# Kernel tuning notes

Hardware: AMD Instinct MI355X
Metric: run time of the kernel (lower is better)

Reference implementation:

```python
import jax, jax.numpy as jnp
import numpy as np

N_NODES = 50000
N_EDGES = 800000


def _gcn_conv(x, W, b, src, dst, deg_inv_sqrt, n_nodes):
    # PyG GCNConv: h = x @ W, then symmetric-normalized sum aggregation
    h = x @ W  # [N, F_out]
    norm = deg_inv_sqrt[src] * deg_inv_sqrt[dst]  # [E_aug]
    msg = h[src] * norm[:, None]  # [E_aug, F_out]
    out = jax.ops.segment_sum(msg, dst, num_segments=n_nodes)
    return out + b


def setup_inputs() -> dict:
    key = jax.random.key(0)
    k1, k2, k3, k4 = jax.random.split(key, 4)
    x = jax.random.normal(k1, (N_NODES, 128), dtype=jnp.float32)
    edge_index = jax.random.randint(k2, (2, N_EDGES), 0, N_NODES, dtype=jnp.int64)
    W1 = jax.random.normal(k3, (128, 64), dtype=jnp.float32) * (1.0 / np.sqrt(128))
    b1 = jnp.zeros((64,), dtype=jnp.float32)
    W2 = jax.random.normal(k4, (64, 32), dtype=jnp.float32) * (1.0 / np.sqrt(64))
    b2 = jnp.zeros((32,), dtype=jnp.float32)
    return {"x": x, "edge_index": edge_index, "W1": W1, "b1": b1, "W2": W2, "b2": b2}


def reference(x, edge_index, W1, b1, W2, b2):
    n_nodes = x.shape[0]
    # add self-loops (PyG GCNConv default)
    loop = jnp.arange(n_nodes, dtype=edge_index.dtype)
    src = jnp.concatenate([edge_index[0], loop])
    dst = jnp.concatenate([edge_index[1], loop])
    # symmetric normalization: deg from target index (gcn_norm)
    deg = jax.ops.segment_sum(jnp.ones_like(dst, dtype=x.dtype), dst, num_segments=n_nodes)
    deg_inv_sqrt = jnp.where(deg > 0, jax.lax.rsqrt(jnp.maximum(deg, 1.0)), 0.0)

    h = _gcn_conv(x, W1, b1, src, dst, deg_inv_sqrt, n_nodes)
    h = jax.nn.relu(h)
    # dropout is identity in eval mode (reference runs inference)
    out = _gcn_conv(h, W2, b2, src, dst, deg_inv_sqrt, n_nodes)
    return out
```

## Files before the change

### kernel.cpp

```cpp
#include <hip/hip_runtime.h>
#include <hip/hip_fp16.h>


#define F_IN 128
#define F_MID 64
#define F_OUT 32
#define NBLK 512
#define NGRP 8
#define SUBCAP 1024
#define CAP 8192
#define CAPN 64

#define RFL(x) __builtin_amdgcn_readfirstlane(x)

__device__ __forceinline__ void h8acc(float* a, const uint4& v) {
    const __half2* hp = (const __half2*)&v;
#pragma unroll
    for (int i = 0; i < 4; ++i) {
        float2 f = __half22float2(hp[i]);
        a[2 * i]     += f.x;
        a[2 * i + 1] += f.y;
    }
}

__device__ __forceinline__ void h8unpack(float* f, const uint4& v) {
    const __half2* hp = (const __half2*)&v;
#pragma unroll
    for (int i = 0; i < 4; ++i) {
        float2 t = __half22float2(hp[i]);
        f[2 * i]     = t.x;
        f[2 * i + 1] = t.y;
    }
}

__device__ __forceinline__ uint4 pack8(const float4& a, const float4& b) {
    union { uint4 u; __half2 h[4]; } pk;
    pk.h[0] = __float22half2_rn(make_float2(a.x, a.y));
    pk.h[1] = __float22half2_rn(make_float2(a.z, a.w));
    pk.h[2] = __float22half2_rn(make_float2(b.x, b.y));
    pk.h[3] = __float22half2_rn(make_float2(b.z, b.w));
    return pk.u;
}

__global__ __launch_bounds__(256, 4) void k_build_gemm1(
    const int* __restrict__ src, const int* __restrict__ dst, int E, int chunk,
    int nbuk, int* __restrict__ cursor, int* __restrict__ esort,
    const float* __restrict__ x, const float* __restrict__ W1,
    float* __restrict__ g1raw, int n) {
    __shared__ float xs[64 * 129];
    int t = threadIdx.x;
    if (blockIdx.x < NBLK) {
        int* cnt = (int*)xs;
        int* off = cnt + 256;
        int* lim = off + 256;
        cnt[t] = 0;
        __syncthreads();
        int e0 = blockIdx.x * chunk;
        int e1 = min(E, e0 + chunk);
        for (int e = e0 + t; e < e1; e += 256)
            atomicAdd(&cnt[dst[e] >> 8], 1);
        __syncthreads();
        int g = blockIdx.x & (NGRP - 1);
        if (t < nbuk) {
            int c = cnt[t];
            int base = t * CAP + g * SUBCAP;
            int r = c ? atomicAdd(&cursor[t * NGRP + g], c) : 0;
            off[t] = base + r;
            lim[t] = base + SUBCAP;
        }
        __syncthreads();
        for (int e = e0 + t; e < e1; e += 256) {
            int d = dst[e];
            int b = d >> 8;
            int pos = atomicAdd(&off[b], 1);
            if (pos < lim[b])
                esort[pos] = (src[e] << 8) | (d & 255);
        }
        return;
    }
    int row0 = (blockIdx.x - NBLK) * 64;
    for (int i = t; i < 64 * (F_IN / 4); i += 256) {
        int r = i >> 5, k4 = i & 31;
        int gr = row0 + r;
        float4 v = make_float4(0.f, 0.f, 0.f, 0.f);
        if (gr < n) v = ((const float4*)x)[(size_t)gr * 32 + k4];
        float* p = &xs[r * 129 + k4 * 4];
        p[0] = v.x; p[1] = v.y; p[2] = v.z; p[3] = v.w;
    }
    __syncthreads();
    int w = RFL(t >> 6);
    int r = t & 63;
    const float4* W4 = (const float4*)W1;
    float4 a0 = {0.f,0.f,0.f,0.f}, a1 = a0, a2 = a0, a3 = a0;
#pragma unroll 4
    for (int k = 0; k < F_IN; ++k) {
        float xv = xs[r * 129 + k];
        float4 w0 = W4[k * 16 + w * 4 + 0];
        float4 w1 = W4[k * 16 + w * 4 + 1];
        float4 w2 = W4[k * 16 + w * 4 + 2];
        float4 w3 = W4[k * 16 + w * 4 + 3];
        a0.x += xv * w0.x; a0.y += xv * w0.y; a0.z += xv * w0.z; a0.w += xv * w0.w;
        a1.x += xv * w1.x; a1.y += xv * w1.y; a1.z += xv * w1.z; a1.w += xv * w1.w;
        a2.x += xv * w2.x; a2.y += xv * w2.y; a2.z += xv * w2.z; a2.w += xv * w2.w;
        a3.x += xv * w3.x; a3.y += xv * w3.y; a3.z += xv * w3.z; a3.w += xv * w3.w;
    }
    int gr = row0 + r;
    if (gr < n) {
        float4* G = (float4*)g1raw;
        size_t base = (size_t)gr * 16 + w * 4;
        G[base + 0] = a0; G[base + 1] = a1; G[base + 2] = a2; G[base + 3] = a3;
    }
}

__global__ __launch_bounds__(256) void k_bucket_pad_scale(
    const int* __restrict__ esort, const int* __restrict__ cursor, int n,
    int* __restrict__ deg, int* __restrict__ elist,
    const float* __restrict__ g1raw, uint4* __restrict__ g1h) {
    __shared__ int cur[256];
    int b = blockIdx.x;
    int t = threadIdx.x;
    int node0 = b << 8;
    cur[t] = 0;
    __syncthreads();
#pragma unroll
    for (int g = 0; g < NGRP; ++g) {
        int c = min(cursor[b * NGRP + g], SUBCAP);
        int s0 = b * CAP + g * SUBCAP;
        for (int e = s0 + t; e < s0 + c; e += 256) {
            int p = esort[e];
            int local = p & 255;
            int pos = atomicAdd(&cur[local], 1);
            if (pos < CAPN)
                elist[((node0 + local) << 6) + pos] = p >> 8;
        }
    }
    __syncthreads();
    int node = node0 + t;
    if (node < n) {
        int dg = cur[t];
        deg[node] = dg;
        int padto = dg < 32 ? 32 : min(CAPN, (dg + 7) & ~7);
        for (int p = dg; p < padto; ++p)
            elist[(node << 6) + p] = node;
    }
    for (int i = t; i < 256 * 8; i += 256) {
        int nl = i >> 3, q = i & 7;
        int nd = node0 + nl;
        if (nd < n) {
            float dv = rsqrtf((float)(cur[nl] + 1));
            const float4* G = (const float4*)g1raw + (size_t)nd * 16 + q * 2;
            float4 u = G[0], v = G[1];
            u.x *= dv; u.y *= dv; u.z *= dv; u.w *= dv;
            v.x *= dv; v.y *= dv; v.z *= dv; v.w *= dv;
            g1h[(size_t)nd * 8 + q] = pack8(u, v);
        }
    }
}

__global__ __launch_bounds__(256) void k_gather1(
    const int* __restrict__ deg, const int* __restrict__ elist,
    const uint4* __restrict__ g1h, const float* __restrict__ b1,
    uint4* __restrict__ h16, int n) {
    int wave = RFL(threadIdx.x >> 6);
    int lane = threadIdx.x & 63;
    int q    = lane & 7;
    int slot = lane >> 3;
    int d    = blockIdx.x * 4 + wave;
    if (d >= n) return;
    int base = d << 6;
    int rawdeg = deg[d];
    int s0 = elist[base + slot];
    int s1 = elist[base + 8 + slot];
    int s2 = elist[base + 16 + slot];
    int s3 = elist[base + 24 + slot];
    uint4 v0 = g1h[(size_t)s0 * 8 + q];
    uint4 v1 = g1h[(size_t)s1 * 8 + q];
    uint4 v2 = g1h[(size_t)s2 * 8 + q];
    uint4 v3 = g1h[(size_t)s3 * 8 + q];
    rawdeg = RFL(rawdeg);
    int cnt = min(rawdeg, CAPN);
    float a[8] = {0,0,0,0,0,0,0,0};
    float b[8] = {0,0,0,0,0,0,0,0};
    if (slot == 0) {
        uint4 v = g1h[(size_t)d * 8 + q];
        h8acc(a, v);
    }
    if (slot < cnt)      h8acc(a, v0);
    if (8 + slot < cnt)  h8acc(b, v1);
    if (16 + slot < cnt) h8acc(a, v2);
    if (24 + slot < cnt) h8acc(b, v3);
    if (cnt > 32) {
        int j = 32;
        for (; j + 8 <= cnt; j += 8) {
            int s = elist[base + j + slot];
            uint4 v = g1h[(size_t)s * 8 + q];
            h8acc(a, v);
        }
        if (slot < cnt - j) {
            int s = elist[base + j + slot];
            uint4 v = g1h[(size_t)s * 8 + q];
            h8acc(a, v);
        }
    }
#pragma unroll
    for (int i = 0; i < 8; ++i) a[i] += b[i];
#pragma unroll
    for (int i = 0; i < 8; ++i) a[i] += __shfl_xor(a[i], 8);
#pragma unroll
    for (int i = 0; i < 8; ++i) a[i] += __shfl_xor(a[i], 16);
#pragma unroll
    for (int i = 0; i < 8; ++i) a[i] += __shfl_xor(a[i], 32);
    if (slot == 0) {
        float dv = rsqrtf((float)(rawdeg + 1));
        float4 bv0 = ((const float4*)b1)[q * 2 + 0];
        float4 bv1 = ((const float4*)b1)[q * 2 + 1];
        float4 o0, o1;
        o0.x = fmaxf(a[0] * dv + bv0.x, 0.f);
        o0.y = fmaxf(a[1] * dv + bv0.y, 0.f);
        o0.z = fmaxf(a[2] * dv + bv0.z, 0.f);
        o0.w = fmaxf(a[3] * dv + bv0.w, 0.f);
        o1.x = fmaxf(a[4] * dv + bv1.x, 0.f);
        o1.y = fmaxf(a[5] * dv + bv1.y, 0.f);
        o1.z = fmaxf(a[6] * dv + bv1.z, 0.f);
        o1.w = fmaxf(a[7] * dv + bv1.w, 0.f);
        h16[(size_t)d * 8 + q] = pack8(o0, o1);
    }
}

__global__ __launch_bounds__(256, 4) void k_gemm2(
    const uint4* __restrict__ h16, const float* __restrict__ W2,
    const int* __restrict__ deg, uint4* __restrict__ g2h, int n) {
    __shared__ float hs[64 * 65];
    int tid  = threadIdx.x;
    int row0 = blockIdx.x * 64;
    for (int i = tid; i < 64 * 8; i += 256) {
        int r = i >> 3, q = i & 7;
        int gr = row0 + r;
        float f[8] = {0,0,0,0,0,0,0,0};
        if (gr < n) {
            uint4 v = h16[(size_t)gr * 8 + q];
            h8unpack(f, v);
        }
        float* p = &hs[r * 65 + q * 8];
#pragma unroll
        for (int k = 0; k < 8; ++k) p[k] = f[k];
    }
    __syncthreads();
    int w = RFL(tid >> 6);
    int r = tid & 63;
    const float4* W4 = (const float4*)W2;
    float4 a0 = {0.f,0.f,0.f,0.f}, a1 = a0;
#pragma unroll 4
    for (int k = 0; k < F_MID; ++k) {
        float hv = hs[r * 65 + k];
        float4 w0 = W4[k * 8 + w * 2 + 0];
        float4 w1 = W4[k * 8 + w * 2 + 1];
        a0.x += hv * w0.x; a0.y += hv * w0.y; a0.z += hv * w0.z; a0.w += hv * w0.w;
        a1.x += hv * w1.x; a1.y += hv * w1.y; a1.z += hv * w1.z; a1.w += hv * w1.w;
    }
    int gr = row0 + r;
    if (gr < n) {
        float dv = rsqrtf((float)(deg[gr] + 1));
        a0.x *= dv; a0.y *= dv; a0.z *= dv; a0.w *= dv;
        a1.x *= dv; a1.y *= dv; a1.z *= dv; a1.w *= dv;
        g2h[(size_t)gr * 4 + w] = pack8(a0, a1);
    }
}

__global__ __launch_bounds__(256) void k_gather2(
    const int* __restrict__ deg, const int* __restrict__ elist,
    const uint4* __restrict__ g2h, const float* __restrict__ b2,
    float* __restrict__ out, int n) {
    int wave = RFL(threadIdx.x >> 6);
    int lane = threadIdx.x & 63;
    int q    = lane & 3;
    int slot = lane >> 2;
    int d    = blockIdx.x * 4 + wave;
    if (d >= n) return;
    int base = d << 6;
    int rawdeg = deg[d];
    int s0 = elist[base + slot];
    int s1 = elist[base + 16 + slot];
    uint4 v0 = g2h[(size_t)s0 * 4 + q];
    uint4 v1 = g2h[(size_t)s1 * 4 + q];
    rawdeg = RFL(rawdeg);
    int cnt = min(rawdeg, CAPN);
    float a[8] = {0,0,0,0,0,0,0,0};
    float b[8] = {0,0,0,0,0,0,0,0};
    if (slot == 0) {
        uint4 v = g2h[(size_t)d * 4 + q];
        h8acc(a, v);
    }
    if (slot < cnt)      h8acc(a, v0);
    if (16 + slot < cnt) h8acc(b, v1);
    if (cnt > 32) {
        int j = 32;
        for (; j + 16 <= cnt; j += 16) {
            int s = elist[base + j + slot];
            uint4 v = g2h[(size_t)s * 4 + q];
            h8acc(a, v);
        }
        if (slot < cnt - j) {
            int s = elist[base + j + slot];
            uint4 v = g2h[(size_t)s * 4 + q];
            h8acc(a, v);
        }
    }
#pragma unroll
    for (int i = 0; i < 8; ++i) a[i] += b[i];
#pragma unroll
    for (int i = 0; i < 8; ++i) a[i] += __shfl_xor(a[i], 4);
#pragma unroll
    for (int i = 0; i < 8; ++i) a[i] += __shfl_xor(a[i], 8);
#pragma unroll
    for (int i = 0; i < 8; ++i) a[i] += __shfl_xor(a[i], 16);
#pragma unroll
    for (int i = 0; i < 8; ++i) a[i] += __shfl_xor(a[i], 32);
    if (slot == 0) {
        float dv = rsqrtf((float)(rawdeg + 1));
        float4 bv0 = ((const float4*)b2)[q * 2 + 0];
        float4 bv1 = ((const float4*)b2)[q * 2 + 1];
        float4 o0, o1;
        o0.x = a[0] * dv + bv0.x;
        o0.y = a[1] * dv + bv0.y;
        o0.z = a[2] * dv + bv0.z;
        o0.w = a[3] * dv + bv0.w;
        o1.x = a[4] * dv + bv1.x;
        o1.y = a[5] * dv + bv1.y;
        o1.z = a[6] * dv + bv1.z;
        o1.w = a[7] * dv + bv1.w;
        float4* O4 = (float4*)out;
        O4[(size_t)d * 8 + q * 2 + 0] = o0;
        O4[(size_t)d * 8 + q * 2 + 1] = o1;
    }
}

extern "C" void kernel_launch(void* const* d_in, const int* in_sizes, int n_in,
                              void* d_out, int out_size, void* d_ws, size_t ws_size,
                              hipStream_t stream) {
    const float* x  = (const float*)d_in[0];
    const int*   ei = (const int*)d_in[1];
    const float* W1 = (const float*)d_in[2];
    const float* b1 = (const float*)d_in[3];
    const float* W2 = (const float*)d_in[4];
    const float* b2 = (const float*)d_in[5];

    int n = in_sizes[0] / F_IN;
    int E = in_sizes[1] / 2;
    const int* src = ei;
    const int* dst = ei + E;

    int nbuk  = (n + 255) >> 8;
    int chunk = (E + NBLK - 1) / NBLK;
    int ngemm = (n + 63) / 64;

    char* ws = (char*)d_ws;
    size_t off = 0;
    auto alloc = [&](size_t bytes) {
        char* p = ws + off;
        off += (bytes + 255) & ~(size_t)255;
        return p;
    };
    int*   cursor = (int*)  alloc((size_t)nbuk * NGRP * 4);
    int*   esort  = (int*)  alloc((size_t)nbuk * CAP * 4);
    int*   deg    = (int*)  alloc((size_t)n * 4);
    int*   elist  = (int*)  alloc((size_t)n * CAPN * 4);
    uint4* g1h    = (uint4*)alloc((size_t)n * F_MID * 2);
    size_t raw_bytes = (size_t)n * F_MID * 4;
    size_t hb        = (size_t)n * F_MID * 2;
    size_t g2b       = (size_t)n * F_OUT * 2;
    char*  region = alloc(raw_bytes > hb + g2b ? raw_bytes : hb + g2b);
    float* g1raw  = (float*)region;
    uint4* h16    = (uint4*)region;
    uint4* g2h    = (uint4*)(region + hb);

    hipMemsetAsync(cursor, 0, (size_t)nbuk * NGRP * 4, stream);
    k_build_gemm1<<<NBLK + ngemm, 256, 0, stream>>>(
        src, dst, E, chunk, nbuk, cursor, esort, x, W1, g1raw, n);
    k_bucket_pad_scale<<<nbuk, 256, 0, stream>>>(
        esort, cursor, n, deg, elist, g1raw, g1h);

    k_gather1<<<(n + 3) / 4, 256, 0, stream>>>(deg, elist, g1h, b1, h16, n);
    k_gemm2<<<(n + 63) / 64, 256, 0, stream>>>(h16, W2, deg, g2h, n);
    k_gather2<<<(n + 3) / 4, 256, 0, stream>>>(deg, elist, g2h, b2,
                                               (float*)d_out, n);
}
```

Measured before the change: 169.0 us.

## Move source-degree scaling into gathers and write fp16 GEMM1 output directly

GEMM1 now writes its fp16 output directly, so the fp32 intermediate round trip and the rescale pass in the bucket kernel go away. The source-side degree normalisation moves into both gather kernels, which load deg[src] per edge and apply an rsqrt-weighted FMA. GEMM2 no longer scales its output. The edge-bucketing blocks also stage packed edges in shared memory between the two passes, though the second pass still rereads dst. The cost is extra random deg loads and rsqrt per edge in the gathers.

Result: no change. 167.1 us (-1.1%).

```diff
diff --git a/kernel.cpp b/kernel.cpp
--- a/kernel.cpp
+++ b/kernel.cpp
@@ -10,16 +10,17 @@
 #define SUBCAP 1024
 #define CAP 8192
 #define CAPN 64
+#define EBUF 1664
 
 #define RFL(x) __builtin_amdgcn_readfirstlane(x)
 
-__device__ __forceinline__ void h8acc(float* a, const uint4& v) {
+__device__ __forceinline__ void h8fma(float* a, const uint4& v, float w) {
     const __half2* hp = (const __half2*)&v;
 #pragma unroll
     for (int i = 0; i < 4; ++i) {
         float2 f = __half22float2(hp[i]);
-        a[2 * i]     += f.x;
-        a[2 * i + 1] += f.y;
+        a[2 * i]     += w * f.x;
+        a[2 * i + 1] += w * f.y;
     }
 }
 
@@ -46,19 +47,30 @@
     const int* __restrict__ src, const int* __restrict__ dst, int E, int chunk,
     int nbuk, int* __restrict__ cursor, int* __restrict__ esort,
     const float* __restrict__ x, const float* __restrict__ W1,
-    float* __restrict__ g1raw, int n) {
+    uint4* __restrict__ g1h, int n) {
     __shared__ float xs[64 * 129];
     int t = threadIdx.x;
     if (blockIdx.x < NBLK) {
-        int* cnt = (int*)xs;
-        int* off = cnt + 256;
-        int* lim = off + 256;
+        int* cnt  = (int*)xs;
+        int* off  = cnt + 256;
+        int* lim  = off + 256;
+        int* ebuf = lim + 256;
         cnt[t] = 0;
         __syncthreads();
         int e0 = blockIdx.x * chunk;
         int e1 = min(E, e0 + chunk);
-        for (int e = e0 + t; e < e1; e += 256)
-            atomicAdd(&cnt[dst[e] >> 8], 1);
+        int ne = e1 - e0;
+        bool staged = (ne <= EBUF);
+        if (staged) {
+            for (int e = e0 + t; e < e1; e += 256) {
+                int d = dst[e];
+                ebuf[e - e0] = (src[e] << 8) | (d & 255);
+                atomicAdd(&cnt[d >> 8], 1);
+            }
+        } else {
+            for (int e = e0 + t; e < e1; e += 256)
+                atomicAdd(&cnt[dst[e] >> 8], 1);
+        }
         __syncthreads();
         int g = blockIdx.x & (NGRP - 1);
         if (t < nbuk) {
@@ -69,12 +81,25 @@
             lim[t] = base + SUBCAP;
         }
         __syncthreads();
-        for (int e = e0 + t; e < e1; e += 256) {
-            int d = dst[e];
-            int b = d >> 8;
-            int pos = atomicAdd(&off[b], 1);
-            if (pos < lim[b])
-                esort[pos] = (src[e] << 8) | (d & 255);
+        if (staged) {
+            for (int i = t; i < ne; i += 256) {
+                int p = ebuf[i];
+                int b = (dst[0], p) ? 0 : 0;
+                b = (unsigned)p & 255;
+                (void)b;
+                int d = dst[e0 + i];
+                int bu = d >> 8;
+                int pos = atomicAdd(&off[bu], 1);
+                if (pos < lim[bu]) esort[pos] = p;
+            }
+        } else {
+            for (int e = e0 + t; e < e1; e += 256) {
+                int d = dst[e];
+                int b = d >> 8;
+                int pos = atomicAdd(&off[b], 1);
+                if (pos < lim[b])
+                    esort[pos] = (src[e] << 8) | (d & 255);
+            }
         }
         return;
     }
@@ -106,16 +131,14 @@
     }
     int gr = row0 + r;
     if (gr < n) {
-        float4* G = (float4*)g1raw;
-        size_t base = (size_t)gr * 16 + w * 4;
-        G[base + 0] = a0; G[base + 1] = a1; G[base + 2] = a2; G[base + 3] = a3;
-    }
-}
-
-__global__ __launch_bounds__(256) void k_bucket_pad_scale(
+        g1h[(size_t)gr * 8 + w * 2 + 0] = pack8(a0, a1);
+        g1h[(size_t)gr * 8 + w * 2 + 1] = pack8(a2, a3);
+    }
+}
+
+__global__ __launch_bounds__(256) void k_bucket_pad(
     const int* __restrict__ esort, const int* __restrict__ cursor, int n,
-    int* __restrict__ deg, int* __restrict__ elist,
-    const float* __restrict__ g1raw, uint4* __restrict__ g1h) {
+    int* __restrict__ deg, int* __restrict__ elist) {
     __shared__ int cur[256];
     int b = blockIdx.x;
     int t = threadIdx.x;
@@ -142,18 +165,6 @@
         int padto = dg < 32 ? 32 : min(CAPN, (dg + 7) & ~7);
         for (int p = dg; p < padto; ++p)
             elist[(node << 6) + p] = node;
-    }
-    for (int i = t; i < 256 * 8; i += 256) {
-        int nl = i >> 3, q = i & 7;
-        int nd = node0 + nl;
-        if (nd < n) {
-            float dv = rsqrtf((float)(cur[nl] + 1));
-            const float4* G = (const float4*)g1raw + (size_t)nd * 16 + q * 2;
-            float4 u = G[0], v = G[1];
-            u.x *= dv; u.y *= dv; u.z *= dv; u.w *= dv;
-            v.x *= dv; v.y *= dv; v.z *= dv; v.w *= dv;
-            g1h[(size_t)nd * 8 + q] = pack8(u, v);
-        }
     }
 }
 
@@ -173,33 +184,38 @@
     int s1 = elist[base + 8 + slot];
     int s2 = elist[base + 16 + slot];
     int s3 = elist[base + 24 + slot];
+    int dg0 = deg[s0];
+    int dg1 = deg[s1];
+    int dg2 = deg[s2];
+    int dg3 = deg[s3];
     uint4 v0 = g1h[(size_t)s0 * 8 + q];
     uint4 v1 = g1h[(size_t)s1 * 8 + q];
     uint4 v2 = g1h[(size_t)s2 * 8 + q];
     uint4 v3 = g1h[(size_t)s3 * 8 + q];
     rawdeg = RFL(rawdeg);
     int cnt = min(rawdeg, CAPN);
+    float dvd = rsqrtf((float)(rawdeg + 1));
     float a[8] = {0,0,0,0,0,0,0,0};
     float b[8] = {0,0,0,0,0,0,0,0};
     if (slot == 0) {
         uint4 v = g1h[(size_t)d * 8 + q];
-        h8acc(a, v);
-    }
-    if (slot < cnt)      h8acc(a, v0);
-    if (8 + slot < cnt)  h8acc(b, v1);
-    if (16 + slot < cnt) h8acc(a, v2);
-    if (24 + slot < cnt) h8acc(b, v3);
+        h8fma(a, v, dvd);
+    }
+    if (slot < cnt)      h8fma(a, v0, rsqrtf((float)(dg0 + 1)));
+    if (8 + slot < cnt)  h8fma(b, v1, rsqrtf((float)(dg1 + 1)));
+    if (16 + slot < cnt) h8fma(a, v2, rsqrtf((float)(dg2 + 1)));
+    if (24 + slot < cnt) h8fma(b, v3, rsqrtf((float)(dg3 + 1)));
     if (cnt > 32) {
         int j = 32;
         for (; j + 8 <= cnt; j += 8) {
             int s = elist[base + j + slot];
             uint4 v = g1h[(size_t)s * 8 + q];
-            h8acc(a, v);
+            h8fma(a, v, rsqrtf((float)(deg[s] + 1)));
         }
         if (slot < cnt - j) {
             int s = elist[base + j + slot];
             uint4 v = g1h[(size_t)s * 8 + q];
-            h8acc(a, v);
+            h8fma(a, v, rsqrtf((float)(deg[s] + 1)));
         }
     }
 #pragma unroll
@@ -211,25 +227,24 @@
 #pragma unroll
     for (int i = 0; i < 8; ++i) a[i] += __shfl_xor(a[i], 32);
     if (slot == 0) {
-        float dv = rsqrtf((float)(rawdeg + 1));
         float4 bv0 = ((const float4*)b1)[q * 2 + 0];
         float4 bv1 = ((const float4*)b1)[q * 2 + 1];
         float4 o0, o1;
-        o0.x = fmaxf(a[0] * dv + bv0.x, 0.f);
-        o0.y = fmaxf(a[1] * dv + bv0.y, 0.f);
-        o0.z = fmaxf(a[2] * dv + bv0.z, 0.f);
-        o0.w = fmaxf(a[3] * dv + bv0.w, 0.f);
-        o1.x = fmaxf(a[4] * dv + bv1.x, 0.f);
-        o1.y = fmaxf(a[5] * dv + bv1.y, 0.f);
-        o1.z = fmaxf(a[6] * dv + bv1.z, 0.f);
-        o1.w = fmaxf(a[7] * dv + bv1.w, 0.f);
+        o0.x = fmaxf(a[0] * dvd + bv0.x, 0.f);
+        o0.y = fmaxf(a[1] * dvd + bv0.y, 0.f);
+        o0.z = fmaxf(a[2] * dvd + bv0.z, 0.f);
+        o0.w = fmaxf(a[3] * dvd + bv0.w, 0.f);
+        o1.x = fmaxf(a[4] * dvd + bv1.x, 0.f);
+        o1.y = fmaxf(a[5] * dvd + bv1.y, 0.f);
+        o1.z = fmaxf(a[6] * dvd + bv1.z, 0.f);
+        o1.w = fmaxf(a[7] * dvd + bv1.w, 0.f);
         h16[(size_t)d * 8 + q] = pack8(o0, o1);
     }
 }
 
 __global__ __launch_bounds__(256, 4) void k_gemm2(
     const uint4* __restrict__ h16, const float* __restrict__ W2,
-    const int* __restrict__ deg, uint4* __restrict__ g2h, int n) {
+    uint4* __restrict__ g2h, int n) {
     __shared__ float hs[64 * 65];
     int tid  = threadIdx.x;
     int row0 = blockIdx.x * 64;
@@ -259,12 +274,8 @@
         a1.x += hv * w1.x; a1.y += hv * w1.y; a1.z += hv * w1.z; a1.w += hv * w1.w;
     }
     int gr = row0 + r;
-    if (gr < n) {
-        float dv = rsqrtf((float)(deg[gr] + 1));
-        a0.x *= dv; a0.y *= dv; a0.z *= dv; a0.w *= dv;
-        a1.x *= dv; a1.y *= dv; a1.z *= dv; a1.w *= dv;
+    if (gr < n)
         g2h[(size_t)gr * 4 + w] = pack8(a0, a1);
-    }
 }
 
 __global__ __launch_bounds__(256) void k_gather2(
@@ -281,29 +292,32 @@
     int rawdeg = deg[d];
     int s0 = elist[base + slot];
     int s1 = elist[base + 16 + slot];
+    int dg0 = deg[s0];
+    int dg1 = deg[s1];
     uint4 v0 = g2h[(size_t)s0 * 4 + q];
     uint4 v1 = g2h[(size_t)s1 * 4 + q];
     rawdeg = RFL(rawdeg);
     int cnt = min(rawdeg, CAPN);
+    float dvd = rsqrtf((float)(rawdeg + 1));
     float a[8] = {0,0,0,0,0,0,0,0};
     float b[8] = {0,0,0,0,0,0,0,0};
     if (slot == 0) {
         uint4 v = g2h[(size_t)d * 4 + q];
-        h8acc(a, v);
-    }
-    if (slot < cnt)      h8acc(a, v0);
-    if (16 + slot < cnt) h8acc(b, v1);
+        h8fma(a, v, dvd);
+    }
+    if (slot < cnt)      h8fma(a, v0, rsqrtf((float)(dg0 + 1)));
+    if (16 + slot < cnt) h8fma(b, v1, rsqrtf((float)(dg1 + 1)));
     if (cnt > 32) {
         int j = 32;
         for (; j + 16 <= cnt; j += 16) {
             int s = elist[base + j + slot];
             uint4 v = g2h[(size_t)s * 4 + q];
-            h8acc(a, v);
+            h8fma(a, v, rsqrtf((float)(deg[s] + 1)));
         }
         if (slot < cnt - j) {
             int s = elist[base + j + slot];
             uint4 v = g2h[(size_t)s * 4 + q];
-            h8acc(a, v);
+            h8fma(a, v, rsqrtf((float)(deg[s] + 1)));
         }
     }
 #pragma unroll
@@ -317,18 +331,17 @@
 #pragma unroll
     for (int i = 0; i < 8; ++i) a[i] += __shfl_xor(a[i], 32);
     if (slot == 0) {
-        float dv = rsqrtf((float)(rawdeg + 1));
         float4 bv0 = ((const float4*)b2)[q * 2 + 0];
         float4 bv1 = ((const float4*)b2)[q * 2 + 1];
         float4 o0, o1;
-        o0.x = a[0] * dv + bv0.x;
-        o0.y = a[1] * dv + bv0.y;
-        o0.z = a[2] * dv + bv0.z;
-        o0.w = a[3] * dv + bv0.w;
-        o1.x = a[4] * dv + bv1.x;
-        o1.y = a[5] * dv + bv1.y;
-        o1.z = a[6] * dv + bv1.z;
-        o1.w = a[7] * dv + bv1.w;
+        o0.x = a[0] * dvd + bv0.x;
+        o0.y = a[1] * dvd + bv0.y;
+        o0.z = a[2] * dvd + bv0.z;
+        o0.w = a[3] * dvd + bv0.w;
+        o1.x = a[4] * dvd + bv1.x;
+        o1.y = a[5] * dvd + bv1.y;
+        o1.z = a[6] * dvd + bv1.z;
+        o1.w = a[7] * dvd + bv1.w;
         float4* O4 = (float4*)out;
         O4[(size_t)d * 8 + q * 2 + 0] = o0;
         O4[(size_t)d * 8 + q * 2 + 1] = o1;
@@ -366,22 +379,16 @@
     int*   deg    = (int*)  alloc((size_t)n * 4);
     int*   elist  = (int*)  alloc((size_t)n * CAPN * 4);
     uint4* g1h    = (uint4*)alloc((size_t)n * F_MID * 2);
-    size_t raw_bytes = (size_t)n * F_MID * 4;
-    size_t hb        = (size_t)n * F_MID * 2;
-    size_t g2b       = (size_t)n * F_OUT * 2;
-    char*  region = alloc(raw_bytes > hb + g2b ? raw_bytes : hb + g2b);
-    float* g1raw  = (float*)region;
-    uint4* h16    = (uint4*)region;
-    uint4* g2h    = (uint4*)(region + hb);
+    uint4* h16    = (uint4*)alloc((size_t)n * F_MID * 2);
+    uint4* g2h    = (uint4*)alloc((size_t)n * F_OUT * 2);
 
     hipMemsetAsync(cursor, 0, (size_t)nbuk * NGRP * 4, stream);
     k_build_gemm1<<<NBLK + ngemm, 256, 0, stream>>>(
-        src, dst, E, chunk, nbuk, cursor, esort, x, W1, g1raw, n);
-    k_bucket_pad_scale<<<nbuk, 256, 0, stream>>>(
-        esort, cursor, n, deg, elist, g1raw, g1h);
+        src, dst, E, chunk, nbuk, cursor, esort, x, W1, g1h, n);
+    k_bucket_pad<<<nbuk, 256, 0, stream>>>(esort, cursor, n, deg, elist);
 
     k_gather1<<<(n + 3) / 4, 256, 0, stream>>>(deg, elist, g1h, b1, h16, n);
-    k_gemm2<<<(n + 63) / 64, 256, 0, stream>>>(h16, W2, deg, g2h, n);
+    k_gemm2<<<(n + 63) / 64, 256, 0, stream>>>(h16, W2, g2h, n);
     k_gather2<<<(n + 3) / 4, 256, 0, stream>>>(deg, elist, g2h, b2,
                                                (float*)d_out, n);
 }
```
